# Kernel tuning notes

Hardware: AMD Instinct MI355X
Metric: run time of the kernel (lower is better)

The kernel has to match this reference:

```python
import jax, jax.numpy as jnp
import numpy as np

N_NODES = 30000
N_EDGES = 480000
F_IN = 64
F_EDGE = 16
HID = 128
N_LAYERS = 3
N_CLASSES = 10
MSG_EPS = 1e-7   # GENConv eps added after ReLU
SM_EPS = 1e-16   # PyG softmax denom eps
LN_EPS = 1e-5


def _layer_norm(x, g, b):
    m = jnp.mean(x, axis=-1, keepdims=True)
    v = jnp.mean((x - m) ** 2, axis=-1, keepdims=True)
    return (x - m) * jax.lax.rsqrt(v + LN_EPS) * g + b


def _gen_conv(h, ea, src, dst, t, w1, b1, lg, lb, w2, b2):
    # GENConv message: relu(x_j + e_ij) + eps  -> [E, H]
    msg = jax.nn.relu(h[src] + ea) + MSG_EPS
    # learnable-temperature segment softmax over incoming edges of each node
    logits = msg * t
    mx = jax.ops.segment_max(logits, dst, num_segments=N_NODES)
    e = jnp.exp(logits - mx[dst])
    s = jax.ops.segment_sum(e, dst, num_segments=N_NODES)
    alpha = e / (s[dst] + SM_EPS)
    agg = jax.ops.segment_sum(msg * alpha, dst, num_segments=N_NODES)  # [N, H]
    # out = MLP(aggr + x): Linear(H,2H) -> LayerNorm -> ReLU -> Linear(2H,H)
    z = agg + h
    z = jax.nn.relu(_layer_norm(z @ w1 + b1, lg, lb)) @ w2 + b2
    return z


def setup_inputs() -> dict:
    key = jax.random.key(0)
    ks = jax.random.split(key, 10)
    g = lambda k, s, sc=0.05: jax.random.normal(k, s, jnp.float32) * sc
    return {
        "x": g(ks[0], (N_NODES, F_IN), 1.0),
        "edge_attr": g(ks[1], (N_EDGES, F_EDGE), 1.0),
        "node_enc_w": g(ks[2], (F_IN, HID)),
        "node_enc_b": jnp.zeros((HID,), jnp.float32),
        "edge_enc_w": g(ks[3], (F_EDGE, HID)),
        "edge_enc_b": jnp.zeros((HID,), jnp.float32),
        "mlp1_w": g(ks[4], (N_LAYERS, HID, 2 * HID)),
        "mlp1_b": jnp.zeros((N_LAYERS, 2 * HID), jnp.float32),
        "mlp_ln_g": jnp.ones((N_LAYERS, 2 * HID), jnp.float32),
        "mlp_ln_b": jnp.zeros((N_LAYERS, 2 * HID), jnp.float32),
        "mlp2_w": g(ks[5], (N_LAYERS, 2 * HID, HID)),
        "mlp2_b": jnp.zeros((N_LAYERS, HID), jnp.float32),
        "t": jnp.ones((N_LAYERS,), jnp.float32),
        "norm_g": jnp.ones((N_LAYERS, HID), jnp.float32),
        "norm_b": jnp.zeros((N_LAYERS, HID), jnp.float32),
        "lin_w": g(ks[6], (HID, N_CLASSES)),
        "lin_b": jnp.zeros((N_CLASSES,), jnp.float32),
        "edge_index": jax.random.randint(ks[7], (2, N_EDGES), 0, N_NODES, jnp.int32),
    }


def reference(x, edge_attr, node_enc_w, node_enc_b, edge_enc_w, edge_enc_b,
              mlp1_w, mlp1_b, mlp_ln_g, mlp_ln_b, mlp2_w, mlp2_b, t,
              norm_g, norm_b, lin_w, lin_b, edge_index):
    src, dst = edge_index[0], edge_index[1]
    ea = edge_attr @ edge_enc_w + edge_enc_b   # [E, H]
    h = x @ node_enc_w + node_enc_b            # [N, H]
    # first layer applies the conv directly (as in the original forward)
    h = _gen_conv(h, ea, src, dst, t[0], mlp1_w[0], mlp1_b[0],
                  mlp_ln_g[0], mlp_ln_b[0], mlp2_w[0], mlp2_b[0])
    # remaining DeepGCN res+ layers: h = h + conv(dropout(relu(norm(h))))
    for i in range(1, N_LAYERS):
        res = h
        z = jax.nn.relu(_layer_norm(h, norm_g[i], norm_b[i]))  # dropout p=0.1 -> identity in eval
        z = _gen_conv(z, ea, src, dst, t[i], mlp1_w[i], mlp1_b[i],
                      mlp_ln_g[i], mlp_ln_b[i], mlp2_w[i], mlp2_b[i])
        h = z + res
    # final norm/act from layers[0] then classifier (dropout -> identity in eval)
    h = jax.nn.relu(_layer_norm(h, norm_g[0], norm_b[0]))
    return h @ lin_w + lin_b
```

## Files before the change

kernel.cpp:

```cpp
#include <hip/hip_runtime.h>
#include <hip/hip_bf16.h>

#define NN 30000
#define NE 480000
#define NROWT 1875

typedef __attribute__((ext_vector_type(8))) short short8;
typedef __attribute__((ext_vector_type(4))) float floatx4;

__device__ __forceinline__ short f2bs(float f) {
    __hip_bfloat16 h = __float2bfloat16(f);
    return *reinterpret_cast<short*>(&h);
}

__device__ __forceinline__ short2 split_bf16(float f) {
    __hip_bfloat16 h = __float2bfloat16(f);
    float r = f - __bfloat162float(h);
    __hip_bfloat16 l = __float2bfloat16(r);
    short2 out;
    out.x = *reinterpret_cast<short*>(&h);
    out.y = *reinterpret_cast<short*>(&l);
    return out;
}

__global__ void presplit_all(const float* __restrict__ ew, const float* __restrict__ nw,
                             const float* __restrict__ m1w, const float* __restrict__ m2w,
                             const float* __restrict__ lw,
                             short* __restrict__ ew_h, short* __restrict__ ew_l,
                             short* __restrict__ nw_h, short* __restrict__ nw_l,
                             short* __restrict__ m1_h, short* __restrict__ m1_l,
                             short* __restrict__ m2_h, short* __restrict__ m2_l,
                             short* __restrict__ lw_h, short* __restrict__ lw_l)
{
    int i = blockIdx.x * 256 + threadIdx.x;
    if (i < 2048) {
        int k = i >> 7, n = i & 127;
        short2 s = split_bf16(ew[i]);
        ew_h[n * 16 + k] = s.x; ew_l[n * 16 + k] = s.y;
    } else if (i < 10240) {
        int j = i - 2048;
        int k = j >> 7, n = j & 127;
        short2 s = split_bf16(nw[j]);
        nw_h[n * 64 + k] = s.x; nw_l[n * 64 + k] = s.y;
    } else if (i < 108544) {
        int j = i - 10240;
        int l = j >> 15, jj = j & 32767;
        int k = jj >> 8, n = jj & 255;
        short2 s = split_bf16(m1w[j]);
        m1_h[(size_t)l * 32768 + n * 128 + k] = s.x;
        m1_l[(size_t)l * 32768 + n * 128 + k] = s.y;
    } else if (i < 206848) {
        int j = i - 108544;
        int l = j >> 15, jj = j & 32767;
        int k = jj >> 7, n = jj & 127;
        short2 s = split_bf16(m2w[j]);
        m2_h[(size_t)l * 32768 + n * 256 + k] = s.x;
        m2_l[(size_t)l * 32768 + n * 256 + k] = s.y;
    } else if (i < 208896) {
        int j = i - 206848;
        int k = j >> 4, n = j & 15;
        short2 s = (n < 10) ? split_bf16(lw[k * 10 + n]) : short2{0, 0};
        lw_h[n * 128 + k] = s.x; lw_l[n * 128 + k] = s.y;
    }
}

template<int K, int N>
__launch_bounds__(256)
__global__ void gemm_a32(const float* __restrict__ A, const short* __restrict__ Bh,
                         const short* __restrict__ Bl, const float* __restrict__ bias,
                         float* __restrict__ C, unsigned* __restrict__ hp, int total_waves)
{
    int wave = ((blockIdx.x * 256) + threadIdx.x) >> 6;
    if (wave >= total_waves) return;
    constexpr int NT = N / 16;
    const int mt = wave / NT, nt = wave % NT;
    const int lane = threadIdx.x & 63;
    const int l15 = lane & 15, quad = lane >> 4;
    const int row = mt * 16 + l15;
    const int col = nt * 16 + l15;
    floatx4 acc = {0.f, 0.f, 0.f, 0.f};
#pragma unroll
    for (int k0 = 0; k0 < K; k0 += 32) {
        const int kb = k0 + quad * 8;
        short8 ah, al;
        const float* ap = A + (size_t)row * K + kb;
        floatx4 a0 = *(const floatx4*)ap;
        floatx4 a1 = *(const floatx4*)(ap + 4);
#pragma unroll
        for (int j = 0; j < 4; j++) {
            short2 s0 = split_bf16(a0[j]); ah[j] = s0.x; al[j] = s0.y;
            short2 s1 = split_bf16(a1[j]); ah[j + 4] = s1.x; al[j + 4] = s1.y;
        }
        short8 bh = *(const short8*)(Bh + (size_t)col * K + kb);
        short8 bl = *(const short8*)(Bl + (size_t)col * K + kb);
        acc = __builtin_amdgcn_mfma_f32_16x16x32_bf16(ah, bh, acc, 0, 0, 0);
        acc = __builtin_amdgcn_mfma_f32_16x16x32_bf16(al, bh, acc, 0, 0, 0);
        acc = __builtin_amdgcn_mfma_f32_16x16x32_bf16(ah, bl, acc, 0, 0, 0);
    }
    float bv = bias[col];
#pragma unroll
    for (int r = 0; r < 4; r++) {
        int ro = mt * 16 + quad * 4 + r;
        float v = acc[r] + bv;
        C[(size_t)ro * N + col] = v;
        int mb = (int)(unsigned short)f2bs(v);
        int ob = __shfl_xor(mb, 1, 64);
        if ((l15 & 1) == 0)
            hp[(size_t)ro * 64 + nt * 8 + (l15 >> 1)] = (unsigned)mb | ((unsigned)ob << 16);
    }
}

template<int K, int NTOT, int NTW, int NREAL>
__launch_bounds__(256)
__global__ void gemm_s(const short* __restrict__ Ah, const short* __restrict__ Al,
                       const short* __restrict__ Bh, const short* __restrict__ Bl,
                       const float* __restrict__ bias, float* __restrict__ C, int total_waves)
{
    int wave = ((blockIdx.x * 256) + threadIdx.x) >> 6;
    if (wave >= total_waves) return;
    constexpr int NG = NTOT / (16 * NTW);
    const int mt = wave / NG, g = wave % NG;
    const int lane = threadIdx.x & 63;
    const int l15 = lane & 15, quad = lane >> 4;
    const int row = mt * 16 + l15;
    floatx4 acc[NTW];
#pragma unroll
    for (int t = 0; t < NTW; t++) acc[t] = {0.f, 0.f, 0.f, 0.f};
#pragma unroll
    for (int k0 = 0; k0 < K; k0 += 32) {
        const int kb = k0 + quad * 8;
        short8 ah = *(const short8*)(Ah + (size_t)row * K + kb);
        short8 al = *(const short8*)(Al + (size_t)row * K + kb);
#pragma unroll
        for (int t = 0; t < NTW; t++) {
            int col = g * NTW * 16 + t * 16 + l15;
            short8 bh = *(const short8*)(Bh + (size_t)col * K + kb);
            short8 bl = *(const short8*)(Bl + (size_t)col * K + kb);
            acc[t] = __builtin_amdgcn_mfma_f32_16x16x32_bf16(ah, bh, acc[t], 0, 0, 0);
            acc[t] = __builtin_amdgcn_mfma_f32_16x16x32_bf16(al, bh, acc[t], 0, 0, 0);
            acc[t] = __builtin_amdgcn_mfma_f32_16x16x32_bf16(ah, bl, acc[t], 0, 0, 0);
        }
    }
#pragma unroll
    for (int t = 0; t < NTW; t++) {
        int col = g * NTW * 16 + t * 16 + l15;
        if (col < NREAL) {
            float bv = bias[col];
#pragma unroll
            for (int r = 0; r < 4; r++) {
                int ro = mt * 16 + quad * 4 + r;
                C[(size_t)ro * NREAL + col] = acc[t][r] + bv;
            }
        }
    }
}

__launch_bounds__(256)
__global__ void gemm_ea(const float* __restrict__ edge_attr, const int* __restrict__ eidx_csr,
                        const short* __restrict__ Bh, const short* __restrict__ Bl,
                        const float* __restrict__ bias, unsigned* __restrict__ ea4)
{
    __shared__ short tile[2][16][132];
    const int wv = threadIdx.x >> 6;
    const int sub = wv >> 1, g = wv & 1;
    const int lane = threadIdx.x & 63;
    const int l15 = lane & 15, quad = lane >> 4;
    const int p = blockIdx.x * 32 + sub * 16 + l15;
    short8 a;
    if (quad < 2) {
        int e = eidx_csr[p];
        const float* ap = edge_attr + (size_t)e * 16 + quad * 8;
        floatx4 a0 = *(const floatx4*)ap;
        floatx4 a1 = *(const floatx4*)(ap + 4);
#pragma unroll
        for (int j = 0; j < 4; j++) { a[j] = f2bs(a0[j]); a[j + 4] = f2bs(a1[j]); }
    } else {
#pragma unroll
        for (int j = 0; j < 8; j++) a[j] = 0;
    }
    floatx4 acc[4];
#pragma unroll
    for (int t = 0; t < 4; t++) acc[t] = {0.f, 0.f, 0.f, 0.f};
#pragma unroll
    for (int t = 0; t < 4; t++) {
        int col = g * 64 + t * 16 + l15;
        short8 bh, bl;
        if (quad < 2) {
            bh = *(const short8*)(Bh + (size_t)col * 16 + quad * 8);
            bl = *(const short8*)(Bl + (size_t)col * 16 + quad * 8);
        } else {
#pragma unroll
            for (int j = 0; j < 8; j++) { bh[j] = 0; bl[j] = 0; }
        }
        acc[t] = __builtin_amdgcn_mfma_f32_16x16x32_bf16(a, bh, acc[t], 0, 0, 0);
        acc[t] = __builtin_amdgcn_mfma_f32_16x16x32_bf16(a, bl, acc[t], 0, 0, 0);
    }
#pragma unroll
    for (int t = 0; t < 4; t++) {
        int col = g * 64 + t * 16 + l15;
        float bv = bias[col];
#pragma unroll
        for (int r = 0; r < 4; r++)
            tile[sub][quad * 4 + r][col] = f2bs(acc[t][r] + bv);
    }
    __syncthreads();
#pragma unroll
    for (int c = 0; c < 2; c++) {
        int idx = threadIdx.x + 256 * c;
        int o = idx * 16;
        int g4l = o >> 10;
        int lp = (o & 1023) >> 4;
        unsigned u[4];
#pragma unroll
        for (int e = 0; e < 4; e++) {
            int rl = g4l * 4 + e;
            u[e] = *(const unsigned*)&tile[rl >> 4][rl & 15][2 * lp];
        }
        uint4 val = make_uint4(u[0], u[1], u[2], u[3]);
        *(uint4*)((char*)ea4 + (size_t)blockIdx.x * 8192 + o) = val;
    }
}

__global__ void zero_kernel(int* __restrict__ p, int n)
{
    int i = blockIdx.x * 256 + threadIdx.x;
    if (i < n) p[i] = 0;
}

__global__ void hist_kernel(const int* __restrict__ dst, int* __restrict__ count)
{
    int e = blockIdx.x * 256 + threadIdx.x;
    if (e < NE) atomicAdd(count + dst[e], 1);
}

__launch_bounds__(1024)
__global__ void scan_kernel(const int* __restrict__ count, int* __restrict__ rowptr)
{
    __shared__ int part[1024];
    const int t = threadIdx.x;
    const int CH = (NN + 1023) / 1024;
    const int base = t * CH;
    int sum = 0;
    for (int j = 0; j < CH; j++) {
        int idx = base + j;
        if (idx < NN) sum += count[idx];
    }
    part[t] = sum;
    __syncthreads();
    for (int d = 1; d < 1024; d <<= 1) {
        int v = (t >= d) ? part[t - d] : 0;
        __syncthreads();
        part[t] += v;
        __syncthreads();
    }
    int off = (t == 0) ? 0 : part[t - 1];
    for (int j = 0; j < CH; j++) {
        int idx = base + j;
        if (idx < NN) { rowptr[idx] = off; off += count[idx]; }
    }
    if (t == 1023) rowptr[NN] = part[1023];
}

__global__ void scatter_kernel(const int* __restrict__ src, const int* __restrict__ dst,
                               const int* __restrict__ rowptr, int* __restrict__ cursor,
                               int* __restrict__ src_csr, int* __restrict__ eidx_csr)
{
    int e = blockIdx.x * 256 + threadIdx.x;
    if (e >= NE) return;
    int d = dst[e];
    int pos = rowptr[d] + atomicAdd(cursor + d, 1);
    src_csr[pos] = src[e];
    eidx_csr[pos] = e;
}

__device__ __forceinline__ void updm(float hv, float av, float tt, float m,
                                     float& s, float& n)
{
    float g = fmaxf(hv + av, 0.f) + 1e-7f;
    float e = __expf(g * tt) * m;
    s += e;
    n = fmaf(g, e, n);
}

__launch_bounds__(256)
__global__ void agg_kernel(const unsigned* __restrict__ hp, const float* __restrict__ hres,
                           const uint4* __restrict__ ea4q, const int* __restrict__ src_csr,
                           const int* __restrict__ rowptr, const float* __restrict__ tptr,
                           int layer, short* __restrict__ Zh, short* __restrict__ Zl)
{
    int node = (blockIdx.x * 256 + threadIdx.x) >> 6;
    if (node >= NN) return;
    const int lane = threadIdx.x & 63;
    const float tt = tptr[layer];
    const int start = rowptr[node];
    const int end = rowptr[node + 1];
    const int g0 = start >> 2, g1 = (end + 3) >> 2;
    float s0 = 0.f, s1 = 0.f, n0 = 0.f, n1 = 0.f;
    float s0b = 0.f, s1b = 0.f, n0b = 0.f, n1b = 0.f;

#define PROC(GG, S0, S1, N0, N1)                                                   \
    {                                                                              \
        uint4 uu = ea4q[((size_t)(GG) << 6) + lane];                               \
        int4 sv = *(const int4*)(src_csr + 4 * (GG));                              \
        int jb = 4 * (GG);                                                         \
        float m0 = (jb     >= start && jb     < end) ? 1.f : 0.f;                  \
        float m1 = (jb + 1 >= start && jb + 1 < end) ? 1.f : 0.f;                  \
        float m2 = (jb + 2 >= start && jb + 2 < end) ? 1.f : 0.f;                  \
        float m3 = (jb + 3 >= start && jb + 3 < end) ? 1.f : 0.f;                  \
        unsigned ha = hp[(size_t)sv.x * 64 + lane];                                \
        unsigned hb = hp[(size_t)sv.y * 64 + lane];                                \
        unsigned hc = hp[(size_t)sv.z * 64 + lane];                                \
        unsigned hd = hp[(size_t)sv.w * 64 + lane];                                \
        updm(__uint_as_float(ha << 16), __uint_as_float(uu.x << 16), tt, m0, S0, N0); \
        updm(__uint_as_float(ha & 0xffff0000u), __uint_as_float(uu.x & 0xffff0000u), tt, m0, S1, N1); \
        updm(__uint_as_float(hb << 16), __uint_as_float(uu.y << 16), tt, m1, S0, N0); \
        updm(__uint_as_float(hb & 0xffff0000u), __uint_as_float(uu.y & 0xffff0000u), tt, m1, S1, N1); \
        updm(__uint_as_float(hc << 16), __uint_as_float(uu.z << 16), tt, m2, S0, N0); \
        updm(__uint_as_float(hc & 0xffff0000u), __uint_as_float(uu.z & 0xffff0000u), tt, m2, S1, N1); \
        updm(__uint_as_float(hd << 16), __uint_as_float(uu.w << 16), tt, m3, S0, N0); \
        updm(__uint_as_float(hd & 0xffff0000u), __uint_as_float(uu.w & 0xffff0000u), tt, m3, S1, N1); \
    }

    int g = g0;
    for (; g + 2 <= g1; g += 2) {
        PROC(g, s0, s1, n0, n1);
        PROC(g + 1, s0b, s1b, n0b, n1b);
    }
    if (g < g1) PROC(g, s0, s1, n0, n1);
#undef PROC
    s0 += s0b; s1 += s1b; n0 += n0b; n1 += n1b;

    float2 res = ((const float2*)hres)[(size_t)node * 64 + lane];
    float ox = n0 / (s0 + 1e-16f) + res.x;
    float oy = n1 / (s1 + 1e-16f) + res.y;
    short2 sx = split_bf16(ox), sy = split_bf16(oy);
    ((unsigned*)Zh)[(size_t)node * 64 + lane] =
        (unsigned)(unsigned short)sx.x | ((unsigned)(unsigned short)sy.x << 16);
    ((unsigned*)Zl)[(size_t)node * 64 + lane] =
        (unsigned)(unsigned short)sx.y | ((unsigned)(unsigned short)sy.y << 16);
}

template<bool HAS_RES, bool FINAL>
__launch_bounds__(256)
__global__ void mlp_fused(const short* __restrict__ Ah, const short* __restrict__ Al,
                          const short* __restrict__ B1h, const short* __restrict__ B1l,
                          const float* __restrict__ b1, const float* __restrict__ g1,
                          const float* __restrict__ be1,
                          const short* __restrict__ B2h, const short* __restrict__ B2l,
                          const float* __restrict__ b2, const float* __restrict__ res,
                          const float* __restrict__ g2, const float* __restrict__ be2,
                          short* __restrict__ z1h, short* __restrict__ z1l,
                          float* __restrict__ Hout, float* __restrict__ HinOut,
                          unsigned* __restrict__ HP,
                          short* __restrict__ Fh, short* __restrict__ Fl)
{
    __shared__ __align__(16) short lds[32768];
    const int wv = threadIdx.x >> 6;
    const int lane = threadIdx.x & 63;
    const int l15 = lane & 15, quad = lane >> 4;
    const int tile = blockIdx.x * 4 + wv;
    const bool valid = (tile < NROWT);
    const int row = tile * 16 + l15;

    floatx4 acc[16];
#pragma unroll
    for (int t = 0; t < 16; t++) acc[t] = {0.f, 0.f, 0.f, 0.f};
    for (int hf = 0; hf < 2; hf++) {
        __syncthreads();
        {
            const float4* s1p = (const float4*)(B1h + hf * 16384);
            const float4* s2p = (const float4*)(B1l + hf * 16384);
            float4* d = (float4*)lds;
#pragma unroll
            for (int i = 0; i < 8; i++) {
                int t8 = threadIdx.x + 256 * i;
                int col = t8 >> 4, k8 = t8 & 15;
                int unit = col * 16 + (k8 ^ (col & 15));
                d[unit] = s1p[t8];
                d[2048 + unit] = s2p[t8];
            }
        }
        __syncthreads();
        if (valid) {
#pragma unroll
            for (int k0 = 0; k0 < 128; k0 += 32) {
                const int kb = k0 + quad * 8;
                const int kb8 = kb >> 3;
                short8 ah = *(const short8*)(Ah + (size_t)row * 128 + kb);
                short8 al = *(const short8*)(Al + (size_t)row * 128 + kb);
#pragma unroll
                for (int t = 0; t < 8; t++) {
                    int col = t * 16 + l15;
                    int unit = col * 16 + (kb8 ^ (col & 15));
                    const short* bp = lds + unit * 8;
                    short8 bh = *(const short8*)bp;
                    short8 bl = *(const short8*)(bp + 16384);
                    int ti = hf * 8 + t;
                    acc[ti] = __builtin_amdgcn_mfma_f32_16x16x32_bf16(ah, bh, acc[ti], 0, 0, 0);
                    acc[ti] = __builtin_amdgcn_mfma_f32_16x16x32_bf16(al, bh, acc[ti], 0, 0, 0);
                    acc[ti] = __builtin_amdgcn_mfma_f32_16x16x32_bf16(ah, bl, acc[ti], 0, 0, 0);
                }
            }
        }
    }
    if (valid) {
#pragma unroll
        for (int t = 0; t < 16; t++) {
            float bv = b1[t * 16 + l15];
#pragma unroll
            for (int r = 0; r < 4; r++) acc[t][r] += bv;
        }
        float s1[4] = {0.f, 0.f, 0.f, 0.f}, s2[4] = {0.f, 0.f, 0.f, 0.f};
#pragma unroll
        for (int t = 0; t < 16; t++)
#pragma unroll
            for (int r = 0; r < 4; r++) { s1[r] += acc[t][r]; s2[r] += acc[t][r] * acc[t][r]; }
#pragma unroll
        for (int m = 1; m <= 8; m <<= 1)
#pragma unroll
            for (int r = 0; r < 4; r++) {
                s1[r] += __shfl_xor(s1[r], m, 64);
                s2[r] += __shfl_xor(s2[r], m, 64);
            }
        float mean[4], rstd[4];
#pragma unroll
        for (int r = 0; r < 4; r++) {
            mean[r] = s1[r] * (1.f / 256.f);
            float var = s2[r] * (1.f / 256.f) - mean[r] * mean[r];
            rstd[r] = rsqrtf(var + 1e-5f);
        }
#pragma unroll
        for (int t = 0; t < 16; t++) {
            int col = t * 16 + l15;
            float gg = g1[col], bb = be1[col];
#pragma unroll
            for (int r = 0; r < 4; r++) {
                float y = fmaxf((acc[t][r] - mean[r]) * rstd[r] * gg + bb, 0.f);
                short2 sp = split_bf16(y);
                int ro = tile * 16 + quad * 4 + r;
                z1h[(size_t)ro * 256 + col] = sp.x;
                z1l[(size_t)ro * 256 + col] = sp.y;
            }
        }
    }
    floatx4 acc2[8];
#pragma unroll
    for (int t = 0; t < 8; t++) acc2[t] = {0.f, 0.f, 0.f, 0.f};
    for (int hf = 0; hf < 2; hf++) {
        __syncthreads();
        {
            const float4* s1p = (const float4*)(B2h + hf * 16384);
            const float4* s2p = (const float4*)(B2l + hf * 16384);
            float4* d = (float4*)lds;
#pragma unroll
            for (int i = 0; i < 8; i++) {
                int t8 = threadIdx.x + 256 * i;
                int col = t8 >> 5, k8 = t8 & 31;
                int unit = col * 32 + (k8 ^ (col & 15));
                d[unit] = s1p[t8];
                d[2048 + unit] = s2p[t8];
            }
        }
        __syncthreads();
        if (valid) {
#pragma unroll
            for (int k0 = 0; k0 < 256; k0 += 32) {
                const int kb = k0 + quad * 8;
                const int kb8 = kb >> 3;
                short8 zh = *(const short8*)(z1h + (size_t)row * 256 + kb);
                short8 zl = *(const short8*)(z1l + (size_t)row * 256 + kb);
#pragma unroll
                for (int t = 0; t < 4; t++) {
                    int col = t * 16 + l15;
                    int unit = col * 32 + (kb8 ^ (col & 15));
                    const short* bp = lds + unit * 8;
                    short8 bh = *(const short8*)bp;
                    short8 bl = *(const short8*)(bp + 16384);
                    int ti = hf * 4 + t;
                    acc2[ti] = __builtin_amdgcn_mfma_f32_16x16x32_bf16(zh, bh, acc2[ti], 0, 0, 0);
                    acc2[ti] = __builtin_amdgcn_mfma_f32_16x16x32_bf16(zl, bh, acc2[ti], 0, 0, 0);
                    acc2[ti] = __builtin_amdgcn_mfma_f32_16x16x32_bf16(zh, bl, acc2[ti], 0, 0, 0);
                }
            }
        }
    }
    if (valid) {
#pragma unroll
        for (int t = 0; t < 8; t++) {
            int col = t * 16 + l15;
            float bv = b2[col];
#pragma unroll
            for (int r = 0; r < 4; r++) {
                acc2[t][r] += bv;
                if (HAS_RES) {
                    int ro = tile * 16 + quad * 4 + r;
                    acc2[t][r] += res[(size_t)ro * 128 + col];
                }
            }
        }
        float s1[4] = {0.f, 0.f, 0.f, 0.f}, s2[4] = {0.f, 0.f, 0.f, 0.f};
#pragma unroll
        for (int t = 0; t < 8; t++)
#pragma unroll
            for (int r = 0; r < 4; r++) { s1[r] += acc2[t][r]; s2[r] += acc2[t][r] * acc2[t][r]; }
#pragma unroll
        for (int m = 1; m <= 8; m <<= 1)
#pragma unroll
            for (int r = 0; r < 4; r++) {
                s1[r] += __shfl_xor(s1[r], m, 64);
                s2[r] += __shfl_xor(s2[r], m, 64);
            }
        float mean[4], rstd[4];
#pragma unroll
        for (int r = 0; r < 4; r++) {
            mean[r] = s1[r] * (1.f / 128.f);
            float var = s2[r] * (1.f / 128.f) - mean[r] * mean[r];
            rstd[r] = rsqrtf(var + 1e-5f);
        }
#pragma unroll
        for (int t = 0; t < 8; t++) {
            int col = t * 16 + l15;
            float gg = g2[col], bb = be2[col];
#pragma unroll
            for (int r = 0; r < 4; r++) {
                int ro = tile * 16 + quad * 4 + r;
                float x = acc2[t][r];
                float y = fmaxf((x - mean[r]) * rstd[r] * gg + bb, 0.f);
                if (FINAL) {
                    short2 sp = split_bf16(y);
                    Fh[(size_t)ro * 128 + col] = sp.x;
                    Fl[(size_t)ro * 128 + col] = sp.y;
                } else {
                    Hout[(size_t)ro * 128 + col] = x;
                    HinOut[(size_t)ro * 128 + col] = y;
                    int yb = (int)(unsigned short)f2bs(y);
                    int ob = __shfl_xor(yb, 1, 64);
                    if ((l15 & 1) == 0)
                        HP[(size_t)ro * 64 + t * 8 + (l15 >> 1)] =
                            (unsigned)yb | ((unsigned)ob << 16);
                }
            }
        }
    }
}

extern "C" void kernel_launch(void* const* d_in, const int* in_sizes, int n_in,
                              void* d_out, int out_size, void* d_ws, size_t ws_size,
                              hipStream_t stream)
{
    const float* x         = (const float*)d_in[0];
    const float* edge_attr = (const float*)d_in[1];
    const float* nw        = (const float*)d_in[2];
    const float* nb        = (const float*)d_in[3];
    const float* ew        = (const float*)d_in[4];
    const float* eb        = (const float*)d_in[5];
    const float* m1w       = (const float*)d_in[6];
    const float* m1b       = (const float*)d_in[7];
    const float* lng       = (const float*)d_in[8];
    const float* lnb       = (const float*)d_in[9];
    const float* m2w       = (const float*)d_in[10];
    const float* m2b       = (const float*)d_in[11];
    const float* tpr       = (const float*)d_in[12];
    const float* ng        = (const float*)d_in[13];
    const float* nbb       = (const float*)d_in[14];
    const float* lw        = (const float*)d_in[15];
    const float* lb        = (const float*)d_in[16];
    const int* ei  = (const int*)d_in[17];
    const int* src = ei;
    const int* dst = ei + NE;

    char* w = (char*)d_ws;
    unsigned* ea4 = (unsigned*)w; w += (size_t)NE * 128 * 2;
    int* src_csr  = (int*)w; w += (size_t)NE * 4;
    int* eidx_csr = (int*)w; w += (size_t)NE * 4;
    unsigned* hp  = (unsigned*)w; w += (size_t)NN * 64 * 4;
    float* h   = (float*)w; w += (size_t)NN * 128 * 4;
    float* hin = (float*)w; w += (size_t)NN * 128 * 4;
    short* zbuf_h = (short*)w; w += (size_t)NN * 128 * 2;
    short* zbuf_l = (short*)w; w += (size_t)NN * 128 * 2;
    short* fin_h  = (short*)w; w += (size_t)NN * 128 * 2;
    short* fin_l  = (short*)w; w += (size_t)NN * 128 * 2;
    short* z1s_h  = (short*)w; w += (size_t)NN * 256 * 2;
    short* z1s_l  = (short*)w; w += (size_t)NN * 256 * 2;
    short* ew_h = (short*)w; w += (size_t)128 * 16 * 2;
    short* ew_l = (short*)w; w += (size_t)128 * 16 * 2;
    short* nw_h = (short*)w; w += (size_t)128 * 64 * 2;
    short* nw_l = (short*)w; w += (size_t)128 * 64 * 2;
    short* m1_h = (short*)w; w += (size_t)3 * 256 * 128 * 2;
    short* m1_l = (short*)w; w += (size_t)3 * 256 * 128 * 2;
    short* m2_h = (short*)w; w += (size_t)3 * 128 * 256 * 2;
    short* m2_l = (short*)w; w += (size_t)3 * 128 * 256 * 2;
    short* lw_h = (short*)w; w += (size_t)16 * 128 * 2;
    short* lw_l = (short*)w; w += (size_t)16 * 128 * 2;
    int* count  = (int*)w;   w += (size_t)NN * 4;
    int* cursor = (int*)w;   w += (size_t)NN * 4;
    int* rowptr = (int*)w;   w += (size_t)(NN + 1) * 4;

    zero_kernel<<<(2 * NN + 255) / 256, 256, 0, stream>>>(count, 2 * NN);
    hist_kernel<<<(NE + 255) / 256, 256, 0, stream>>>(dst, count);
    scan_kernel<<<1, 1024, 0, stream>>>(count, rowptr);
    scatter_kernel<<<(NE + 255) / 256, 256, 0, stream>>>(src, dst, rowptr, cursor,
                                                         src_csr, eidx_csr);

    presplit_all<<<(208896 + 255) / 256, 256, 0, stream>>>(
        ew, nw, m1w, m2w, lw, ew_h, ew_l, nw_h, nw_l, m1_h, m1_l, m2_h, m2_l, lw_h, lw_l);

    gemm_ea<<<NE / 32, 256, 0, stream>>>(edge_attr, eidx_csr, ew_h, ew_l, eb, ea4);
    gemm_a32<64, 128><<<(NN / 16) * 8 / 4, 256, 0, stream>>>(x, nw_h, nw_l, nb, h, hp,
                                                             (NN / 16) * 8);

    const uint4* ea4q = (const uint4*)ea4;
    const int mgrid = (NROWT + 3) / 4;
    for (int layer = 0; layer < 3; ++layer) {
        const float* hi = (layer == 0) ? h : hin;
        agg_kernel<<<NN / 4, 256, 0, stream>>>(hp, hi, ea4q, src_csr, rowptr, tpr, layer,
                                               zbuf_h, zbuf_l);
        if (layer == 0) {
            mlp_fused<false, false><<<mgrid, 256, 0, stream>>>(
                zbuf_h, zbuf_l, m1_h, m1_l, m1b, lng, lnb,
                m2_h, m2_l, m2b, nullptr, ng + 128, nbb + 128,
                z1s_h, z1s_l, h, hin, hp, nullptr, nullptr);
        } else if (layer == 1) {
            mlp_fused<true, false><<<mgrid, 256, 0, stream>>>(
                zbuf_h, zbuf_l, m1_h + 32768, m1_l + 32768, m1b + 256, lng + 256, lnb + 256,
                m2_h + 32768, m2_l + 32768, m2b + 128, h, ng + 256, nbb + 256,
                z1s_h, z1s_l, h, hin, hp, nullptr, nullptr);
        } else {
            mlp_fused<true, true><<<mgrid, 256, 0, stream>>>(
                zbuf_h, zbuf_l, m1_h + 65536, m1_l + 65536, m1b + 512, lng + 512, lnb + 512,
                m2_h + 65536, m2_l + 65536, m2b + 256, h, ng, nbb,
                z1s_h, z1s_l, nullptr, nullptr, nullptr, fin_h, fin_l);
        }
    }
    gemm_s<128, 16, 1, 10><<<((NN / 16) + 3) / 4, 256, 0, stream>>>(
        fin_h, fin_l, lw_h, lw_l, lb, (float*)d_out, NN / 16);
}
```

Measured before the change: 507.9 us.

## Fuse edge-encoder GEMM into aggregation kernel, recomputing edge features per layer

Removes the precomputed bf16 edge-embedding buffer (480K x 128) and the separate gemm_ea launch. Each aggregation wavefront now gathers raw 16-float edge attributes for up to 16 incoming edges, runs MFMA against the edge weight, and stages the bf16 result in LDS. The goal is to avoid writing that buffer once and reading it three times. In exchange the edge GEMM is recomputed in every layer, only the high bf16 part of the weight is used (lower precision than the previous hi/lo split), and shuffles, LDS traffic and a serial per-edge loop are added.

```diff
diff --git a/kernel.cpp b/kernel.cpp
--- a/kernel.cpp
+++ b/kernel.cpp
@@ -155,72 +155,6 @@
     }
 }
 
-__launch_bounds__(256)
-__global__ void gemm_ea(const float* __restrict__ edge_attr, const int* __restrict__ eidx_csr,
-                        const short* __restrict__ Bh, const short* __restrict__ Bl,
-                        const float* __restrict__ bias, unsigned* __restrict__ ea4)
-{
-    __shared__ short tile[2][16][132];
-    const int wv = threadIdx.x >> 6;
-    const int sub = wv >> 1, g = wv & 1;
-    const int lane = threadIdx.x & 63;
-    const int l15 = lane & 15, quad = lane >> 4;
-    const int p = blockIdx.x * 32 + sub * 16 + l15;
-    short8 a;
-    if (quad < 2) {
-        int e = eidx_csr[p];
-        const float* ap = edge_attr + (size_t)e * 16 + quad * 8;
-        floatx4 a0 = *(const floatx4*)ap;
-        floatx4 a1 = *(const floatx4*)(ap + 4);
-#pragma unroll
-        for (int j = 0; j < 4; j++) { a[j] = f2bs(a0[j]); a[j + 4] = f2bs(a1[j]); }
-    } else {
-#pragma unroll
-        for (int j = 0; j < 8; j++) a[j] = 0;
-    }
-    floatx4 acc[4];
-#pragma unroll
-    for (int t = 0; t < 4; t++) acc[t] = {0.f, 0.f, 0.f, 0.f};
-#pragma unroll
-    for (int t = 0; t < 4; t++) {
-        int col = g * 64 + t * 16 + l15;
-        short8 bh, bl;
-        if (quad < 2) {
-            bh = *(const short8*)(Bh + (size_t)col * 16 + quad * 8);
-            bl = *(const short8*)(Bl + (size_t)col * 16 + quad * 8);
-        } else {
-#pragma unroll
-            for (int j = 0; j < 8; j++) { bh[j] = 0; bl[j] = 0; }
-        }
-        acc[t] = __builtin_amdgcn_mfma_f32_16x16x32_bf16(a, bh, acc[t], 0, 0, 0);
-        acc[t] = __builtin_amdgcn_mfma_f32_16x16x32_bf16(a, bl, acc[t], 0, 0, 0);
-    }
-#pragma unroll
-    for (int t = 0; t < 4; t++) {
-        int col = g * 64 + t * 16 + l15;
-        float bv = bias[col];
-#pragma unroll
-        for (int r = 0; r < 4; r++)
-            tile[sub][quad * 4 + r][col] = f2bs(acc[t][r] + bv);
-    }
-    __syncthreads();
-#pragma unroll
-    for (int c = 0; c < 2; c++) {
-        int idx = threadIdx.x + 256 * c;
-        int o = idx * 16;
-        int g4l = o >> 10;
-        int lp = (o & 1023) >> 4;
-        unsigned u[4];
-#pragma unroll
-        for (int e = 0; e < 4; e++) {
-            int rl = g4l * 4 + e;
-            u[e] = *(const unsigned*)&tile[rl >> 4][rl & 15][2 * lp];
-        }
-        uint4 val = make_uint4(u[0], u[1], u[2], u[3]);
-        *(uint4*)((char*)ea4 + (size_t)blockIdx.x * 8192 + o) = val;
-    }
-}
-
 __global__ void zero_kernel(int* __restrict__ p, int n)
 {
     int i = blockIdx.x * 256 + threadIdx.x;
@@ -273,61 +207,97 @@
     eidx_csr[pos] = e;
 }
 
-__device__ __forceinline__ void updm(float hv, float av, float tt, float m,
-                                     float& s, float& n)
+__device__ __forceinline__ void upd(float hv, float av, float tt, float& s, float& n)
 {
     float g = fmaxf(hv + av, 0.f) + 1e-7f;
-    float e = __expf(g * tt) * m;
+    float e = __expf(g * tt);
     s += e;
     n = fmaf(g, e, n);
 }
 
 __launch_bounds__(256)
 __global__ void agg_kernel(const unsigned* __restrict__ hp, const float* __restrict__ hres,
-                           const uint4* __restrict__ ea4q, const int* __restrict__ src_csr,
-                           const int* __restrict__ rowptr, const float* __restrict__ tptr,
-                           int layer, short* __restrict__ Zh, short* __restrict__ Zl)
-{
+                           const float* __restrict__ edge_attr,
+                           const int* __restrict__ eidx_csr, const int* __restrict__ src_csr,
+                           const int* __restrict__ rowptr,
+                           const short* __restrict__ ewh, const float* __restrict__ ebias,
+                           const float* __restrict__ tptr, int layer,
+                           short* __restrict__ Zh, short* __restrict__ Zl)
+{
+    __shared__ unsigned lds[4][64 * 17];
+    const int wv = threadIdx.x >> 6;
+    unsigned* reg = lds[wv];
     int node = (blockIdx.x * 256 + threadIdx.x) >> 6;
     if (node >= NN) return;
     const int lane = threadIdx.x & 63;
+    const int l15 = lane & 15, quad = lane >> 4;
     const float tt = tptr[layer];
+    short8 bf[8];
+#pragma unroll
+    for (int t = 0; t < 8; t++) {
+        if (quad < 2) bf[t] = *(const short8*)(ewh + (size_t)(t * 16 + l15) * 16 + quad * 8);
+        else {
+#pragma unroll
+            for (int j = 0; j < 8; j++) bf[t][j] = 0;
+        }
+    }
+    float bt[8];
+#pragma unroll
+    for (int t = 0; t < 8; t++) bt[t] = ebias[t * 16 + l15];
+
     const int start = rowptr[node];
     const int end = rowptr[node + 1];
-    const int g0 = start >> 2, g1 = (end + 3) >> 2;
     float s0 = 0.f, s1 = 0.f, n0 = 0.f, n1 = 0.f;
     float s0b = 0.f, s1b = 0.f, n0b = 0.f, n1b = 0.f;
 
-#define PROC(GG, S0, S1, N0, N1)                                                   \
-    {                                                                              \
-        uint4 uu = ea4q[((size_t)(GG) << 6) + lane];                               \
-        int4 sv = *(const int4*)(src_csr + 4 * (GG));                              \
-        int jb = 4 * (GG);                                                         \
-        float m0 = (jb     >= start && jb     < end) ? 1.f : 0.f;                  \
-        float m1 = (jb + 1 >= start && jb + 1 < end) ? 1.f : 0.f;                  \
-        float m2 = (jb + 2 >= start && jb + 2 < end) ? 1.f : 0.f;                  \
-        float m3 = (jb + 3 >= start && jb + 3 < end) ? 1.f : 0.f;                  \
-        unsigned ha = hp[(size_t)sv.x * 64 + lane];                                \
-        unsigned hb = hp[(size_t)sv.y * 64 + lane];                                \
-        unsigned hc = hp[(size_t)sv.z * 64 + lane];                                \
-        unsigned hd = hp[(size_t)sv.w * 64 + lane];                                \
-        updm(__uint_as_float(ha << 16), __uint_as_float(uu.x << 16), tt, m0, S0, N0); \
-        updm(__uint_as_float(ha & 0xffff0000u), __uint_as_float(uu.x & 0xffff0000u), tt, m0, S1, N1); \
-        updm(__uint_as_float(hb << 16), __uint_as_float(uu.y << 16), tt, m1, S0, N0); \
-        updm(__uint_as_float(hb & 0xffff0000u), __uint_as_float(uu.y & 0xffff0000u), tt, m1, S1, N1); \
-        updm(__uint_as_float(hc << 16), __uint_as_float(uu.z << 16), tt, m2, S0, N0); \
-        updm(__uint_as_float(hc & 0xffff0000u), __uint_as_float(uu.z & 0xffff0000u), tt, m2, S1, N1); \
-        updm(__uint_as_float(hd << 16), __uint_as_float(uu.w << 16), tt, m3, S0, N0); \
-        updm(__uint_as_float(hd & 0xffff0000u), __uint_as_float(uu.w & 0xffff0000u), tt, m3, S1, N1); \
-    }
-
-    int g = g0;
-    for (; g + 2 <= g1; g += 2) {
-        PROC(g, s0, s1, n0, n1);
-        PROC(g + 1, s0b, s1b, n0b, n1b);
-    }
-    if (g < g1) PROC(g, s0, s1, n0, n1);
-#undef PROC
+    for (int gb = start; gb < end; gb += 16) {
+        const int ne = min(16, end - gb);
+        short8 a;
+        if (quad < 2) {
+            int e = eidx_csr[gb + ((l15 < ne) ? l15 : 0)];
+            const float* ap = edge_attr + (size_t)e * 16 + quad * 8;
+            floatx4 a0 = *(const floatx4*)ap;
+            floatx4 a1 = *(const floatx4*)(ap + 4);
+#pragma unroll
+            for (int j = 0; j < 4; j++) { a[j] = f2bs(a0[j]); a[j + 4] = f2bs(a1[j]); }
+        } else {
+#pragma unroll
+            for (int j = 0; j < 8; j++) a[j] = 0;
+        }
+#pragma unroll
+        for (int t = 0; t < 8; t++) {
+            floatx4 d = {0.f, 0.f, 0.f, 0.f};
+            d = __builtin_amdgcn_mfma_f32_16x16x32_bf16(a, bf[t], d, 0, 0, 0);
+#pragma unroll
+            for (int r = 0; r < 4; r++) {
+                float v = d[r] + bt[t];
+                int mb = (int)(unsigned short)f2bs(v);
+                int ob = __shfl_xor(mb, 1, 64);
+                if ((l15 & 1) == 0)
+                    reg[(t * 8 + (l15 >> 1)) * 17 + quad * 4 + r] =
+                        (unsigned)mb | ((unsigned)ob << 16);
+            }
+        }
+        int j = 0;
+        for (; j + 2 <= ne; j += 2) {
+            int sa = src_csr[gb + j], sb = src_csr[gb + j + 1];
+            unsigned ea_a = reg[lane * 17 + j];
+            unsigned ea_b = reg[lane * 17 + j + 1];
+            unsigned ha = hp[(size_t)sa * 64 + lane];
+            unsigned hb = hp[(size_t)sb * 64 + lane];
+            upd(__uint_as_float(ha << 16), __uint_as_float(ea_a << 16), tt, s0, n0);
+            upd(__uint_as_float(ha & 0xffff0000u), __uint_as_float(ea_a & 0xffff0000u), tt, s1, n1);
+            upd(__uint_as_float(hb << 16), __uint_as_float(ea_b << 16), tt, s0b, n0b);
+            upd(__uint_as_float(hb & 0xffff0000u), __uint_as_float(ea_b & 0xffff0000u), tt, s1b, n1b);
+        }
+        if (j < ne) {
+            int sa = src_csr[gb + j];
+            unsigned ea_a = reg[lane * 17 + j];
+            unsigned ha = hp[(size_t)sa * 64 + lane];
+            upd(__uint_as_float(ha << 16), __uint_as_float(ea_a << 16), tt, s0, n0);
+            upd(__uint_as_float(ha & 0xffff0000u), __uint_as_float(ea_a & 0xffff0000u), tt, s1, n1);
+        }
+    }
     s0 += s0b; s1 += s1b; n0 += n0b; n1 += n1b;
 
     float2 res = ((const float2*)hres)[(size_t)node * 64 + lane];
@@ -570,7 +540,6 @@
     const int* dst = ei + NE;
 
     char* w = (char*)d_ws;
-    unsigned* ea4 = (unsigned*)w; w += (size_t)NE * 128 * 2;
     int* src_csr  = (int*)w; w += (size_t)NE * 4;
     int* eidx_csr = (int*)w; w += (size_t)NE * 4;
     unsigned* hp  = (unsigned*)w; w += (size_t)NN * 64 * 4;
@@ -605,15 +574,14 @@
     presplit_all<<<(208896 + 255) / 256, 256, 0, stream>>>(
         ew, nw, m1w, m2w, lw, ew_h, ew_l, nw_h, nw_l, m1_h, m1_l, m2_h, m2_l, lw_h, lw_l);
 
-    gemm_ea<<<NE / 32, 256, 0, stream>>>(edge_attr, eidx_csr, ew_h, ew_l, eb, ea4);
     gemm_a32<64, 128><<<(NN / 16) * 8 / 4, 256, 0, stream>>>(x, nw_h, nw_l, nb, h, hp,
                                                              (NN / 16) * 8);
 
-    const uint4* ea4q = (const uint4*)ea4;
     const int mgrid = (NROWT + 3) / 4;
     for (int layer = 0; layer < 3; ++layer) {
         const float* hi = (layer == 0) ? h : hin;
-        agg_kernel<<<NN / 4, 256, 0, stream>>>(hp, hi, ea4q, src_csr, rowptr, tpr, layer,
+        agg_kernel<<<NN / 4, 256, 0, stream>>>(hp, hi, edge_attr, eidx_csr, src_csr,
+                                               rowptr, ew_h, eb, tpr, layer,
                                                zbuf_h, zbuf_l);
         if (layer == 0) {
             mlp_fused<false, false><<<mgrid, 256, 0, stream>>>(
```

After: 588.8 us. 1.16x slower.
